# Optimization experiments

Hardware: AMD Instinct MI355X
Metric: run time of the kernel (lower is better)

## Reference

```python
import jax, jax.numpy as jnp
import numpy as np

K_SEL = 8        # selection budget K
R_ITER = 1       # fixed-point refinement steps r
LAM = 0.5        # lam
MAX_PROXY = 16   # max_proxy_points
KNN_K = 1        # knn_k = max(1, r)


def knn_stats(x, k):
    # x: [B,N,D] -> [B,N,4] stats of k nearest-neighbor distances (self excluded)
    sq = jnp.sum(x * x, axis=-1)
    d2 = sq[:, :, None] + sq[:, None, :] - 2.0 * jnp.einsum('bnd,bmd->bnm', x, x)
    n = x.shape[1]
    d2 = d2 + jnp.eye(n, dtype=x.dtype) * 1e9  # mask self-distance
    neg_vals, _ = jax.lax.top_k(-d2, k)        # k smallest distances
    d = jnp.sqrt(jnp.maximum(-neg_vals, 0.0))  # [B,N,k]
    return jnp.stack([d.mean(-1), d.min(-1), d.max(-1), d.std(-1)], axis=-1)


def build_structural(x, selection_weights=None, knn_k=KNN_K):
    feats = jnp.concatenate([x, knn_stats(x, knn_k)], axis=-1)
    if selection_weights is not None:
        feats = jnp.concatenate([feats, selection_weights[..., None]], axis=-1)
    return feats


def feature_similarity(f):
    fn = f / (jnp.linalg.norm(f, axis=-1, keepdims=True) + 1e-8)
    return jnp.einsum('bnd,bmd->bnm', fn, fn)


def soft_selector(saliency, similarity, log_temp):
    # SoftSelectorProxy.forward
    temp = jnp.clip(jnp.exp(log_temp), 0.1, 10.0)
    y = jax.nn.sigmoid((saliency / (2.0 * LAM) - 0.5) / temp)

    def rescale(y):
        budget = jnp.clip(y.sum(axis=1, keepdims=True), 1e-6, None)
        return y * jnp.minimum(K_SEL / budget, 1.0)

    y = rescale(y)
    for _ in range(R_ITER):
        overlap = jnp.einsum('bnm,bm->bn', similarity, y)
        y = rescale(y / (1.0 + overlap))
    return y


def setup_inputs() -> dict:
    key = jax.random.key(0)
    ks = jax.random.split(key, 8)
    B, N, D, H = 8, 2048, 32, 64
    K_LIFT, D_MODEL = 16, 256
    ANCHOR = D + 4  # structural_feature_dim(input_dim, include_selection=False)
    s = 0.02
    return {
        'x': jax.random.normal(ks[0], (B, N, D), dtype=jnp.float32),
        'log_temp': jnp.zeros((), dtype=jnp.float32),  # init_temperature=1.0
        'W1': jax.random.normal(ks[1], (D, H), dtype=jnp.float32) * s,
        'b1': jnp.zeros((H,), dtype=jnp.float32),
        'W2': jax.random.normal(ks[2], (H, 1), dtype=jnp.float32) * s,
        'b2': jnp.zeros((1,), dtype=jnp.float32),
        'mu': jnp.zeros((ANCHOR,), dtype=jnp.float32),
        'sigma': jnp.ones((ANCHOR,), dtype=jnp.float32),
        'Wl': jax.random.normal(ks[3], (ANCHOR, K_LIFT), dtype=jnp.float32) * s,
        'bl': jnp.zeros((K_LIFT,), dtype=jnp.float32),
        'Wp': jax.random.normal(ks[4], (K_LIFT, D_MODEL), dtype=jnp.float32) * s,
        'bp': jnp.zeros((D_MODEL,), dtype=jnp.float32),
    }


def reference(x, log_temp, W1, b1, W2, b2, mu, sigma, Wl, bl, Wp, bp):
    # CausalEventModel: per-point MLP saliency head
    h = jax.nn.relu(jnp.einsum('bnd,dh->bnh', x, W1) + b1)
    saliency = (jnp.einsum('bnh,ho->bno', h, W2) + b2)[..., 0]  # [B,N]

    structural = build_structural(x, selection_weights=saliency)
    similarity = feature_similarity(structural)                  # [B,N,N]
    y_star = soft_selector(saliency, similarity, log_temp)       # [B,N]

    dense = build_structural(x, selection_weights=None)          # [B,N,anchor]
    lifted = jnp.tanh(jnp.einsum('bna,ak->bnk', (dense - mu) / sigma, Wl) + bl)

    N = lifted.shape[1]
    K_eff = min(N, MAX_PROXY)
    _, top_idx = jax.lax.top_k(y_star, K_eff)                    # [B,K_eff]
    cloud = jnp.take_along_axis(lifted, top_idx[..., None], axis=1)  # [B,K_eff,k]
    tokens = jnp.einsum('bkc,cd->bkd', cloud, Wp) + bp           # [B,K_eff,d_model]
    return tokens, y_star
```

## Files before the change

### kernel.cpp

```cpp
#include <hip/hip_runtime.h>
#include <math.h>

#define B 8
#define N 2048
#define DIM 32
#define HID 64
#define KLIFT 16
#define DMODEL 256
#define KPROXY 16
#define KSEL 8.0f

typedef float f32x4 __attribute__((ext_vector_type(4)));
typedef short bf16x8 __attribute__((ext_vector_type(8)));

__device__ inline unsigned short f2bf(float f) {
  unsigned u = __float_as_uint(f);
  unsigned r = (u + 0x7FFFu + ((u >> 16) & 1u)) >> 16;
  return (unsigned short)r;
}
__device__ inline float bf2f(unsigned short s) {
  return __uint_as_float(((unsigned)s) << 16);
}
__device__ inline float clip_temp(float lt) {
  return fminf(fmaxf(expf(lt), 0.1f), 10.f);
}

__global__ __launch_bounds__(256) void k_prep(
    const float* __restrict__ x, const float* __restrict__ W1,
    const float* __restrict__ b1, const float* __restrict__ W2,
    const float* __restrict__ b2, const float* __restrict__ logt,
    float* __restrict__ sal, float* __restrict__ sq,
    unsigned short* __restrict__ Xhi, unsigned short* __restrict__ Xlo,
    float* __restrict__ partials1, unsigned* __restrict__ nnd2) {
  __shared__ float sW1[DIM * HID];
  __shared__ float sW2[HID], sb1[HID];
  __shared__ float red[4];
  int t = threadIdx.x;
  int lane = t & 63, wid = t >> 6;
  {
    const float4* s4 = (const float4*)W1;
    float4* d4 = (float4*)sW1;
    for (int i = t; i < DIM * HID / 4; i += 256) d4[i] = s4[i];
    if (t < HID) { sW2[t] = W2[t]; sb1[t] = b1[t]; }
  }
  __syncthreads();
  int p = blockIdx.x * 256 + t;
  nnd2[p] = 0x7F7F7F7Fu;
  float xr[DIM];
  const float4* xp = (const float4*)(x + (size_t)p * DIM);
#pragma unroll
  for (int i = 0; i < DIM / 4; i++) {
    float4 v = xp[i];
    xr[4 * i + 0] = v.x; xr[4 * i + 1] = v.y; xr[4 * i + 2] = v.z; xr[4 * i + 3] = v.w;
  }
  float s = 0.f;
#pragma unroll
  for (int d = 0; d < DIM; d++) s = fmaf(xr[d], xr[d], s);
  sq[p] = s;
  float h[HID];
#pragma unroll
  for (int j = 0; j < HID; j++) h[j] = sb1[j];
  for (int d = 0; d < DIM; d++) {
    float xv = xr[d];
    const float4* wrow = (const float4*)(&sW1[d * HID]);
#pragma unroll
    for (int j4 = 0; j4 < HID / 4; j4++) {
      float4 w = wrow[j4];
      h[4 * j4 + 0] = fmaf(xv, w.x, h[4 * j4 + 0]);
      h[4 * j4 + 1] = fmaf(xv, w.y, h[4 * j4 + 1]);
      h[4 * j4 + 2] = fmaf(xv, w.z, h[4 * j4 + 2]);
      h[4 * j4 + 3] = fmaf(xv, w.w, h[4 * j4 + 3]);
    }
  }
  float acc = b2[0];
#pragma unroll
  for (int j = 0; j < HID; j++) acc = fmaf(fmaxf(h[j], 0.f), sW2[j], acc);
  sal[p] = acc;
  float temp = clip_temp(logt[0]);
  float y0 = 1.f / (1.f + expf(-((acc - 0.5f) / temp)));
  float part = y0;
#pragma unroll
  for (int off = 32; off >= 1; off >>= 1) part += __shfl_xor(part, off);
  if (lane == 0) red[wid] = part;
  __syncthreads();
  if (t == 0) partials1[blockIdx.x] = red[0] + red[1] + red[2] + red[3];
  int bb = p >> 11, n = p & (N - 1);
  int tile = n >> 4, c = n & 15;
  size_t tb = ((size_t)(bb * 128 + tile)) * 64;
#pragma unroll
  for (int g = 0; g < 4; g++) {
    bf16x8 hv, lv;
#pragma unroll
    for (int j = 0; j < 8; j++) {
      float v = xr[g * 8 + j];
      unsigned short hb = f2bf(v);
      hv[j] = (short)hb;
      lv[j] = (short)f2bf(v - bf2f(hb));
    }
    size_t off = (tb + (size_t)g * 16 + c) * 8;
    *(bf16x8*)(Xhi + off) = hv;
    *(bf16x8*)(Xlo + off) = lv;
  }
}

__global__ __launch_bounds__(256) void k_nnd(
    const unsigned short* __restrict__ Xhi, const unsigned short* __restrict__ Xlo,
    const float* __restrict__ sq, unsigned* __restrict__ nnd2) {
  int bid = blockIdx.x;
  int bb = bid >> 7;
  int nch = (bid >> 3) & 15;
  int mo = bid & 7;
  int t = threadIdx.x;
  int w = t >> 6, lane = t & 63;
  int c = lane & 15, g = lane >> 4;
  __shared__ unsigned short ldsH[16 * 512];
  __shared__ unsigned short ldsL[16 * 512];
  __shared__ float ssq[256];
  {
    size_t base = ((size_t)(bb * 128 + mo * 16)) * 512;
    const float4* srcH = (const float4*)(Xhi + base);
    const float4* srcL = (const float4*)(Xlo + base);
    float4* dH = (float4*)ldsH;
    float4* dL = (float4*)ldsL;
    for (int i = t; i < 1024; i += 256) { dH[i] = srcH[i]; dL[i] = srcL[i]; }
    ssq[t] = sq[bb * N + mo * 256 + t];
  }
  int nt0 = nch * 8 + w * 2, nt1 = nt0 + 1;
  bf16x8 ah0 = *(const bf16x8*)(Xhi + (((size_t)(bb * 128 + nt0)) * 64 + lane) * 8);
  bf16x8 al0 = *(const bf16x8*)(Xlo + (((size_t)(bb * 128 + nt0)) * 64 + lane) * 8);
  bf16x8 ah1 = *(const bf16x8*)(Xhi + (((size_t)(bb * 128 + nt1)) * 64 + lane) * 8);
  bf16x8 al1 = *(const bf16x8*)(Xlo + (((size_t)(bb * 128 + nt1)) * 64 + lane) * 8);
  __syncthreads();
  float mn0[4] = {1e30f, 1e30f, 1e30f, 1e30f};
  float mn1[4] = {1e30f, 1e30f, 1e30f, 1e30f};
  for (int tt = 0; tt < 16; tt++) {
    bf16x8 bh = ((const bf16x8*)(ldsH + tt * 512))[lane];
    bf16x8 bl2 = ((const bf16x8*)(ldsL + tt * 512))[lane];
    f32x4 a0 = {0.f, 0.f, 0.f, 0.f};
    f32x4 a1 = {0.f, 0.f, 0.f, 0.f};
    a0 = __builtin_amdgcn_mfma_f32_16x16x32_bf16(ah0, bh, a0, 0, 0, 0);
    a1 = __builtin_amdgcn_mfma_f32_16x16x32_bf16(ah1, bh, a1, 0, 0, 0);
    a0 = __builtin_amdgcn_mfma_f32_16x16x32_bf16(ah0, bl2, a0, 0, 0, 0);
    a1 = __builtin_amdgcn_mfma_f32_16x16x32_bf16(ah1, bl2, a1, 0, 0, 0);
    a0 = __builtin_amdgcn_mfma_f32_16x16x32_bf16(al0, bh, a0, 0, 0, 0);
    a1 = __builtin_amdgcn_mfma_f32_16x16x32_bf16(al1, bh, a1, 0, 0, 0);
    float sm = ssq[tt * 16 + c];
    int mtg = mo * 16 + tt;
    bool d0 = (mtg == nt0), d1 = (mtg == nt1);
#pragma unroll
    for (int r = 0; r < 4; r++) {
      float v0 = fmaf(-2.f, a0[r], sm);
      float v1 = fmaf(-2.f, a1[r], sm);
      if (d0 && c == 4 * g + r) v0 = 1e30f;
      if (d1 && c == 4 * g + r) v1 = 1e30f;
      mn0[r] = fminf(mn0[r], v0);
      mn1[r] = fminf(mn1[r], v1);
    }
  }
#pragma unroll
  for (int off = 1; off <= 8; off <<= 1) {
#pragma unroll
    for (int r = 0; r < 4; r++) {
      mn0[r] = fminf(mn0[r], __shfl_xor(mn0[r], off));
      mn1[r] = fminf(mn1[r], __shfl_xor(mn1[r], off));
    }
  }
  if (c == 0) {
#pragma unroll
    for (int r = 0; r < 4; r++) {
      int n0 = nt0 * 16 + 4 * g + r;
      float v = fmaxf(sq[bb * N + n0] + mn0[r], 0.f);
      atomicMin(&nnd2[bb * N + n0], __float_as_uint(v));
      int n1 = nt1 * 16 + 4 * g + r;
      v = fmaxf(sq[bb * N + n1] + mn1[r], 0.f);
      atomicMin(&nnd2[bb * N + n1], __float_as_uint(v));
    }
  }
}

__global__ __launch_bounds__(256) void k_c1(
    const float* __restrict__ x, const float* __restrict__ sal,
    const float* __restrict__ sq, const unsigned* __restrict__ nnd2,
    const float* __restrict__ logt, const float* __restrict__ partials1,
    float* __restrict__ gpart) {
  int bid = blockIdx.x;
  int bb = bid >> 3, ch = bid & 7;
  int t = threadIdx.x, lane = t & 63, wid = t >> 6;
  __shared__ float xs[256][33];
  __shared__ float cs[256];
  __shared__ float gsh[8][32];
  __shared__ float red32[4], red33[4];
  int n = ch * 256 + t;
  size_t base = (size_t)bb * N + n;
  float temp = clip_temp(logt[0]);
  float b1v = 0.f;
  for (int j = 0; j < 8; j++) b1v += partials1[bb * 8 + j];
  float scale1 = fminf(KSEL / fmaxf(b1v, 1e-6f), 1.f);
  float sv = sal[base];
  float y0 = 1.f / (1.f + expf(-((sv - 0.5f) / temp)));
  float y1 = y0 * scale1;
  float dv = sqrtf(__uint_as_float(nnd2[base]));
  float nrm = sqrtf(sq[base] + 3.f * dv * dv + sv * sv) + 1e-8f;
  float cn = y1 / nrm;
  cs[t] = cn;
  {
    const float4* xsrc = (const float4*)(x + ((size_t)bb * N + ch * 256) * DIM);
    for (int j = t; j < 2048; j += 256) {
      float4 v = xsrc[j];
      int pt = j >> 3, c4 = (j & 7) * 4;
      xs[pt][c4 + 0] = v.x; xs[pt][c4 + 1] = v.y;
      xs[pt][c4 + 2] = v.z; xs[pt][c4 + 3] = v.w;
    }
  }
  float v32 = cn * dv, v33 = cn * sv;
#pragma unroll
  for (int off = 32; off >= 1; off >>= 1) {
    v32 += __shfl_xor(v32, off);
    v33 += __shfl_xor(v33, off);
  }
  if (lane == 0) { red32[wid] = v32; red33[wid] = v33; }
  __syncthreads();
  if (t == 0) {
    gpart[(size_t)(bb * 8 + ch) * 36 + 32] = red32[0] + red32[1] + red32[2] + red32[3];
    gpart[(size_t)(bb * 8 + ch) * 36 + 33] = red33[0] + red33[1] + red33[2] + red33[3];
  }
  int d = t & 31, pg = t >> 5;
  float acc = 0.f;
#pragma unroll
  for (int i = 0; i < 32; i++) acc = fmaf(cs[pg * 32 + i], xs[pg * 32 + i][d], acc);
  gsh[pg][d] = acc;
  __syncthreads();
  if (t < 32) {
    float s = 0.f;
#pragma unroll
    for (int pgi = 0; pgi < 8; pgi++) s += gsh[pgi][t];
    gpart[(size_t)(bb * 8 + ch) * 36 + t] = s;
  }
}

__global__ __launch_bounds__(256) void k_c(
    const float* __restrict__ x, const float* __restrict__ sal,
    const float* __restrict__ sq, const unsigned* __restrict__ nnd2,
    const float* __restrict__ logt, const float* __restrict__ partials1,
    const float* __restrict__ gpart, float* __restrict__ partials2,
    float* __restrict__ y2buf) {
  int bid = blockIdx.x;
  int bb = bid >> 3, ch = bid & 7;
  int t = threadIdx.x, lane = t & 63, wid = t >> 6;
  __shared__ float gfin[34];
  __shared__ float s1sh;
  __shared__ float red[4];
  if (t < 34) {
    float s = 0.f;
    for (int j = 0; j < 8; j++) s += gpart[(size_t)(bb * 8 + j) * 36 + t];
    gfin[t] = s;
  }
  if (t == 40) {
    float s = 0.f;
    for (int j = 0; j < 8; j++) s += partials1[bb * 8 + j];
    s1sh = fminf(KSEL / fmaxf(s, 1e-6f), 1.f);
  }
  __syncthreads();
  float scale1 = s1sh;
  int n = ch * 256 + t;
  size_t base = (size_t)bb * N + n;
  float temp = clip_temp(logt[0]);
  float sv = sal[base];
  float y0 = 1.f / (1.f + expf(-((sv - 0.5f) / temp)));
  float y1 = y0 * scale1;
  float dv = sqrtf(__uint_as_float(nnd2[base]));
  float nrm = sqrtf(sq[base] + 3.f * dv * dv + sv * sv) + 1e-8f;
  const float4* p4 = (const float4*)(x + base * DIM);
  float ov = 0.f;
#pragma unroll
  for (int cc = 0; cc < 8; cc++) {
    float4 v = p4[cc];
    ov = fmaf(v.x, gfin[4 * cc + 0], ov);
    ov = fmaf(v.y, gfin[4 * cc + 1], ov);
    ov = fmaf(v.z, gfin[4 * cc + 2], ov);
    ov = fmaf(v.w, gfin[4 * cc + 3], ov);
  }
  ov += 3.f * dv * gfin[32] + sv * gfin[33];
  ov /= nrm;
  float y2 = y1 / (1.f + ov);
  y2buf[base] = y2;
  float part = y2;
#pragma unroll
  for (int off = 32; off >= 1; off >>= 1) part += __shfl_xor(part, off);
  if (lane == 0) red[wid] = part;
  __syncthreads();
  if (t == 0) partials2[bb * 8 + ch] = red[0] + red[1] + red[2] + red[3];
}

__global__ __launch_bounds__(256) void k_rank(
    const float* __restrict__ y2buf, const float* __restrict__ partials2,
    float* __restrict__ ystar, int* __restrict__ topidx) {
  int bid = blockIdx.x;
  int bb = bid >> 4, seg = bid & 15;
  int t = threadIdx.x;
  __shared__ float yv[N];
  __shared__ float s2sh;
  if (t == 0) {
    float s = 0.f;
    for (int j = 0; j < 8; j++) s += partials2[bb * 8 + j];
    s2sh = fminf(KSEL / fmaxf(s, 1e-6f), 1.f);
  }
  __syncthreads();
  float scale2 = s2sh;
  size_t base = (size_t)bb * N;
  {
    const float4* src = (const float4*)(y2buf + base);
    float4* dst = (float4*)yv;
#pragma unroll
    for (int i = 0; i < 2; i++) {
      float4 v = src[t + 256 * i];
      v.x *= scale2; v.y *= scale2; v.z *= scale2; v.w *= scale2;
      dst[t + 256 * i] = v;
    }
  }
  __syncthreads();
  int pt = seg * 128 + (t >> 1);
  int h = t & 1;
  float vi = yv[pt];
  if (h == 0) ystar[base + pt] = vi;
  int cnt = 0;
  const float4* yv4 = (const float4*)yv;
  int j0 = h * 256;
#define RCMP(a, q4) { int jb = (q4) * 4; \
    cnt += (a.x > vi || (a.x == vi && jb + 0 < pt)); \
    cnt += (a.y > vi || (a.y == vi && jb + 1 < pt)); \
    cnt += (a.z > vi || (a.z == vi && jb + 2 < pt)); \
    cnt += (a.w > vi || (a.w == vi && jb + 3 < pt)); }
  for (int it = 0; it < 32; it++) {
    int jj = j0 + it * 8;
    float4 a0 = yv4[jj + 0]; float4 a1 = yv4[jj + 1];
    float4 a2 = yv4[jj + 2]; float4 a3 = yv4[jj + 3];
    float4 a4 = yv4[jj + 4]; float4 a5 = yv4[jj + 5];
    float4 a6 = yv4[jj + 6]; float4 a7 = yv4[jj + 7];
    RCMP(a0, jj + 0); RCMP(a1, jj + 1); RCMP(a2, jj + 2); RCMP(a3, jj + 3);
    RCMP(a4, jj + 4); RCMP(a5, jj + 5); RCMP(a6, jj + 6); RCMP(a7, jj + 7);
  }
#undef RCMP
  int oc = __shfl_xor(cnt, 1);
  int tot = cnt + oc;
  if (h == 0 && tot < KPROXY) topidx[bb * KPROXY + tot] = pt;
}

__global__ __launch_bounds__(256) void k_tok(
    const float* __restrict__ x, const unsigned* __restrict__ nnd2,
    const int* __restrict__ topidx, const float* __restrict__ mu,
    const float* __restrict__ sigma, const float* __restrict__ Wl,
    const float* __restrict__ bl, const float* __restrict__ Wp,
    const float* __restrict__ bp, float* __restrict__ tok) {
  int bk = blockIdx.x;
  int b = bk >> 4, k = bk & 15;
  int t = threadIdx.x;
  __shared__ float z[36]; __shared__ float lift[KLIFT]; __shared__ int srow;
  if (t == 0) srow = topidx[b * KPROXY + k];
  __syncthreads();
  int n = srow;
  if (t < 36) {
    float dvv;
    if (t < DIM) dvv = x[((size_t)(b * N + n)) * DIM + t];
    else if (t < 35) dvv = sqrtf(__uint_as_float(nnd2[b * N + n]));
    else dvv = 0.f;
    z[t] = (dvv - mu[t]) / sigma[t];
  }
  __syncthreads();
  if (t < KLIFT) {
    float a = bl[t];
#pragma unroll
    for (int d = 0; d < 36; d++) a = fmaf(z[d], Wl[d * KLIFT + t], a);
    lift[t] = tanhf(a);
  }
  __syncthreads();
  float a = bp[t];
#pragma unroll
  for (int j = 0; j < KLIFT; j++) a = fmaf(lift[j], Wp[j * DMODEL + t], a);
  tok[(size_t)(b * KPROXY + k) * DMODEL + t] = a;
}

extern "C" void kernel_launch(void* const* d_in, const int* in_sizes, int n_in,
                              void* d_out, int out_size, void* d_ws, size_t ws_size,
                              hipStream_t stream) {
  const float* x  = (const float*)d_in[0];
  const float* lt = (const float*)d_in[1];
  const float* W1 = (const float*)d_in[2];
  const float* b1 = (const float*)d_in[3];
  const float* W2 = (const float*)d_in[4];
  const float* b2 = (const float*)d_in[5];
  const float* mu = (const float*)d_in[6];
  const float* sg = (const float*)d_in[7];
  const float* Wl = (const float*)d_in[8];
  const float* bl = (const float*)d_in[9];
  const float* Wp = (const float*)d_in[10];
  const float* bp = (const float*)d_in[11];

  float* tok = (float*)d_out;
  float* ystar = tok + B * KPROXY * DMODEL;

  char* ws = (char*)d_ws;
  float* sal          = (float*)(ws);
  float* sq           = (float*)(ws + 65536);
  unsigned* nnd2      = (unsigned*)(ws + 131072);
  float* y2buf        = (float*)(ws + 196608);
  float* partials1    = (float*)(ws + 262144);
  float* gpart        = (float*)(ws + 262656);
  float* partials2    = (float*)(ws + 272384);
  int* topidx         = (int*)(ws + 272896);
  unsigned short* Xhi = (unsigned short*)(ws + 327680);
  unsigned short* Xlo = (unsigned short*)(ws + 327680 + 1048576);

  k_prep<<<B * N / 256, 256, 0, stream>>>(x, W1, b1, W2, b2, lt, sal, sq, Xhi, Xlo, partials1, nnd2);
  k_nnd<<<B * 16 * 8, 256, 0, stream>>>(Xhi, Xlo, sq, nnd2);
  k_c1<<<B * 8, 256, 0, stream>>>(x, sal, sq, nnd2, lt, partials1, gpart);
  k_c<<<B * 8, 256, 0, stream>>>(x, sal, sq, nnd2, lt, partials1, gpart, partials2, y2buf);
  k_rank<<<B * 16, 256, 0, stream>>>(y2buf, partials2, ystar, topidx);
  k_tok<<<B * KPROXY, 256, 0, stream>>>(x, nnd2, topidx, mu, sg, Wl, bl, Wp, bp, tok);
}
```

Baseline: 63.43 us.

## Fuse four tail kernels into one persistent kernel with grid barriers

New measurement: 109.4 us. +72.4%, slower.

```diff
diff --git a/kernel.cpp b/kernel.cpp
--- a/kernel.cpp
+++ b/kernel.cpp
@@ -9,6 +9,7 @@
 #define DMODEL 256
 #define KPROXY 16
 #define KSEL 8.0f
+#define NBLK 64
 
 typedef float f32x4 __attribute__((ext_vector_type(4)));
 typedef short bf16x8 __attribute__((ext_vector_type(8)));
@@ -23,6 +24,17 @@
 }
 __device__ inline float clip_temp(float lt) {
   return fminf(fmaxf(expf(lt), 0.1f), 10.f);
+}
+
+__device__ inline void grid_barrier(unsigned* ctr, int t) {
+  __syncthreads();
+  if (t == 0) {
+    __threadfence();
+    atomicAdd(ctr, 1u);
+    while (atomicAdd(ctr, 0u) < (unsigned)NBLK) __builtin_amdgcn_s_sleep(4);
+    __threadfence();
+  }
+  __syncthreads();
 }
 
 __global__ __launch_bounds__(256) void k_prep(
@@ -31,12 +43,14 @@
     const float* __restrict__ b2, const float* __restrict__ logt,
     float* __restrict__ sal, float* __restrict__ sq,
     unsigned short* __restrict__ Xhi, unsigned short* __restrict__ Xlo,
-    float* __restrict__ partials1, unsigned* __restrict__ nnd2) {
+    float* __restrict__ partials1, unsigned* __restrict__ nnd2,
+    unsigned* __restrict__ barctr) {
   __shared__ float sW1[DIM * HID];
   __shared__ float sW2[HID], sb1[HID];
   __shared__ float red[4];
   int t = threadIdx.x;
   int lane = t & 63, wid = t >> 6;
+  if (blockIdx.x == 0 && t < 4) barctr[t] = 0u;
   {
     const float4* s4 = (const float4*)W1;
     float4* d4 = (float4*)sW1;
@@ -178,206 +192,206 @@
   }
 }
 
-__global__ __launch_bounds__(256) void k_c1(
+__global__ __launch_bounds__(256) void k_tail(
     const float* __restrict__ x, const float* __restrict__ sal,
     const float* __restrict__ sq, const unsigned* __restrict__ nnd2,
     const float* __restrict__ logt, const float* __restrict__ partials1,
-    float* __restrict__ gpart) {
+    float* __restrict__ gpart, float* __restrict__ partials2,
+    float* __restrict__ y2buf, int* __restrict__ topidx,
+    const float* __restrict__ mu, const float* __restrict__ sigma,
+    const float* __restrict__ Wl, const float* __restrict__ bl,
+    const float* __restrict__ Wp, const float* __restrict__ bp,
+    float* __restrict__ ystar, float* __restrict__ tok,
+    unsigned* __restrict__ barctr) {
   int bid = blockIdx.x;
-  int bb = bid >> 3, ch = bid & 7;
   int t = threadIdx.x, lane = t & 63, wid = t >> 6;
   __shared__ float xs[256][33];
   __shared__ float cs[256];
   __shared__ float gsh[8][32];
   __shared__ float red32[4], red33[4];
-  int n = ch * 256 + t;
-  size_t base = (size_t)bb * N + n;
-  float temp = clip_temp(logt[0]);
-  float b1v = 0.f;
-  for (int j = 0; j < 8; j++) b1v += partials1[bb * 8 + j];
-  float scale1 = fminf(KSEL / fmaxf(b1v, 1e-6f), 1.f);
-  float sv = sal[base];
-  float y0 = 1.f / (1.f + expf(-((sv - 0.5f) / temp)));
-  float y1 = y0 * scale1;
-  float dv = sqrtf(__uint_as_float(nnd2[base]));
-  float nrm = sqrtf(sq[base] + 3.f * dv * dv + sv * sv) + 1e-8f;
-  float cn = y1 / nrm;
-  cs[t] = cn;
-  {
-    const float4* xsrc = (const float4*)(x + ((size_t)bb * N + ch * 256) * DIM);
-    for (int j = t; j < 2048; j += 256) {
-      float4 v = xsrc[j];
-      int pt = j >> 3, c4 = (j & 7) * 4;
-      xs[pt][c4 + 0] = v.x; xs[pt][c4 + 1] = v.y;
-      xs[pt][c4 + 2] = v.z; xs[pt][c4 + 3] = v.w;
-    }
-  }
-  float v32 = cn * dv, v33 = cn * sv;
-#pragma unroll
-  for (int off = 32; off >= 1; off >>= 1) {
-    v32 += __shfl_xor(v32, off);
-    v33 += __shfl_xor(v33, off);
-  }
-  if (lane == 0) { red32[wid] = v32; red33[wid] = v33; }
-  __syncthreads();
-  if (t == 0) {
-    gpart[(size_t)(bb * 8 + ch) * 36 + 32] = red32[0] + red32[1] + red32[2] + red32[3];
-    gpart[(size_t)(bb * 8 + ch) * 36 + 33] = red33[0] + red33[1] + red33[2] + red33[3];
-  }
-  int d = t & 31, pg = t >> 5;
-  float acc = 0.f;
-#pragma unroll
-  for (int i = 0; i < 32; i++) acc = fmaf(cs[pg * 32 + i], xs[pg * 32 + i][d], acc);
-  gsh[pg][d] = acc;
-  __syncthreads();
-  if (t < 32) {
-    float s = 0.f;
-#pragma unroll
-    for (int pgi = 0; pgi < 8; pgi++) s += gsh[pgi][t];
-    gpart[(size_t)(bb * 8 + ch) * 36 + t] = s;
-  }
-}
-
-__global__ __launch_bounds__(256) void k_c(
-    const float* __restrict__ x, const float* __restrict__ sal,
-    const float* __restrict__ sq, const unsigned* __restrict__ nnd2,
-    const float* __restrict__ logt, const float* __restrict__ partials1,
-    const float* __restrict__ gpart, float* __restrict__ partials2,
-    float* __restrict__ y2buf) {
-  int bid = blockIdx.x;
-  int bb = bid >> 3, ch = bid & 7;
-  int t = threadIdx.x, lane = t & 63, wid = t >> 6;
   __shared__ float gfin[34];
   __shared__ float s1sh;
   __shared__ float red[4];
-  if (t < 34) {
-    float s = 0.f;
-    for (int j = 0; j < 8; j++) s += gpart[(size_t)(bb * 8 + j) * 36 + t];
-    gfin[t] = s;
-  }
-  if (t == 40) {
-    float s = 0.f;
-    for (int j = 0; j < 8; j++) s += partials1[bb * 8 + j];
-    s1sh = fminf(KSEL / fmaxf(s, 1e-6f), 1.f);
-  }
-  __syncthreads();
-  float scale1 = s1sh;
-  int n = ch * 256 + t;
-  size_t base = (size_t)bb * N + n;
-  float temp = clip_temp(logt[0]);
-  float sv = sal[base];
-  float y0 = 1.f / (1.f + expf(-((sv - 0.5f) / temp)));
-  float y1 = y0 * scale1;
-  float dv = sqrtf(__uint_as_float(nnd2[base]));
-  float nrm = sqrtf(sq[base] + 3.f * dv * dv + sv * sv) + 1e-8f;
-  const float4* p4 = (const float4*)(x + base * DIM);
-  float ov = 0.f;
-#pragma unroll
-  for (int cc = 0; cc < 8; cc++) {
-    float4 v = p4[cc];
-    ov = fmaf(v.x, gfin[4 * cc + 0], ov);
-    ov = fmaf(v.y, gfin[4 * cc + 1], ov);
-    ov = fmaf(v.z, gfin[4 * cc + 2], ov);
-    ov = fmaf(v.w, gfin[4 * cc + 3], ov);
-  }
-  ov += 3.f * dv * gfin[32] + sv * gfin[33];
-  ov /= nrm;
-  float y2 = y1 / (1.f + ov);
-  y2buf[base] = y2;
-  float part = y2;
-#pragma unroll
-  for (int off = 32; off >= 1; off >>= 1) part += __shfl_xor(part, off);
-  if (lane == 0) red[wid] = part;
-  __syncthreads();
-  if (t == 0) partials2[bb * 8 + ch] = red[0] + red[1] + red[2] + red[3];
-}
-
-__global__ __launch_bounds__(256) void k_rank(
-    const float* __restrict__ y2buf, const float* __restrict__ partials2,
-    float* __restrict__ ystar, int* __restrict__ topidx) {
-  int bid = blockIdx.x;
-  int bb = bid >> 4, seg = bid & 15;
-  int t = threadIdx.x;
   __shared__ float yv[N];
   __shared__ float s2sh;
-  if (t == 0) {
-    float s = 0.f;
-    for (int j = 0; j < 8; j++) s += partials2[bb * 8 + j];
-    s2sh = fminf(KSEL / fmaxf(s, 1e-6f), 1.f);
-  }
-  __syncthreads();
-  float scale2 = s2sh;
-  size_t base = (size_t)bb * N;
+  __shared__ float z[36];
+  __shared__ float lift[KLIFT];
+  __shared__ int srow;
+
+  float temp = clip_temp(logt[0]);
+  int bb = bid >> 3, ch = bid & 7;
+
   {
-    const float4* src = (const float4*)(y2buf + base);
-    float4* dst = (float4*)yv;
-#pragma unroll
-    for (int i = 0; i < 2; i++) {
-      float4 v = src[t + 256 * i];
-      v.x *= scale2; v.y *= scale2; v.z *= scale2; v.w *= scale2;
-      dst[t + 256 * i] = v;
-    }
-  }
-  __syncthreads();
-  int pt = seg * 128 + (t >> 1);
-  int h = t & 1;
-  float vi = yv[pt];
-  if (h == 0) ystar[base + pt] = vi;
-  int cnt = 0;
-  const float4* yv4 = (const float4*)yv;
-  int j0 = h * 256;
+    int n = ch * 256 + t;
+    size_t base = (size_t)bb * N + n;
+    float b1v = 0.f;
+    for (int j = 0; j < 8; j++) b1v += partials1[bb * 8 + j];
+    float scale1 = fminf(KSEL / fmaxf(b1v, 1e-6f), 1.f);
+    float sv = sal[base];
+    float y0 = 1.f / (1.f + expf(-((sv - 0.5f) / temp)));
+    float y1 = y0 * scale1;
+    float dv = sqrtf(__uint_as_float(nnd2[base]));
+    float nrm = sqrtf(sq[base] + 3.f * dv * dv + sv * sv) + 1e-8f;
+    float cn = y1 / nrm;
+    cs[t] = cn;
+    {
+      const float4* xsrc = (const float4*)(x + ((size_t)bb * N + ch * 256) * DIM);
+      for (int j = t; j < 2048; j += 256) {
+        float4 v = xsrc[j];
+        int pt = j >> 3, c4 = (j & 7) * 4;
+        xs[pt][c4 + 0] = v.x; xs[pt][c4 + 1] = v.y;
+        xs[pt][c4 + 2] = v.z; xs[pt][c4 + 3] = v.w;
+      }
+    }
+    float v32 = cn * dv, v33 = cn * sv;
+#pragma unroll
+    for (int off = 32; off >= 1; off >>= 1) {
+      v32 += __shfl_xor(v32, off);
+      v33 += __shfl_xor(v33, off);
+    }
+    if (lane == 0) { red32[wid] = v32; red33[wid] = v33; }
+    __syncthreads();
+    if (t == 0) {
+      gpart[(size_t)(bb * 8 + ch) * 36 + 32] = red32[0] + red32[1] + red32[2] + red32[3];
+      gpart[(size_t)(bb * 8 + ch) * 36 + 33] = red33[0] + red33[1] + red33[2] + red33[3];
+    }
+    int d = t & 31, pg = t >> 5;
+    float acc = 0.f;
+#pragma unroll
+    for (int i = 0; i < 32; i++) acc = fmaf(cs[pg * 32 + i], xs[pg * 32 + i][d], acc);
+    gsh[pg][d] = acc;
+    __syncthreads();
+    if (t < 32) {
+      float s = 0.f;
+#pragma unroll
+      for (int pgi = 0; pgi < 8; pgi++) s += gsh[pgi][t];
+      gpart[(size_t)(bb * 8 + ch) * 36 + t] = s;
+    }
+  }
+  grid_barrier(&barctr[0], t);
+
+  {
+    if (t < 34) {
+      float s = 0.f;
+      for (int j = 0; j < 8; j++) s += gpart[(size_t)(bb * 8 + j) * 36 + t];
+      gfin[t] = s;
+    }
+    if (t == 40) {
+      float s = 0.f;
+      for (int j = 0; j < 8; j++) s += partials1[bb * 8 + j];
+      s1sh = fminf(KSEL / fmaxf(s, 1e-6f), 1.f);
+    }
+    __syncthreads();
+    float scale1 = s1sh;
+    int n = ch * 256 + t;
+    size_t base = (size_t)bb * N + n;
+    float sv = sal[base];
+    float y0 = 1.f / (1.f + expf(-((sv - 0.5f) / temp)));
+    float y1 = y0 * scale1;
+    float dv = sqrtf(__uint_as_float(nnd2[base]));
+    float nrm = sqrtf(sq[base] + 3.f * dv * dv + sv * sv) + 1e-8f;
+    const float4* p4 = (const float4*)(x + base * DIM);
+    float ov = 0.f;
+#pragma unroll
+    for (int cc = 0; cc < 8; cc++) {
+      float4 v = p4[cc];
+      ov = fmaf(v.x, gfin[4 * cc + 0], ov);
+      ov = fmaf(v.y, gfin[4 * cc + 1], ov);
+      ov = fmaf(v.z, gfin[4 * cc + 2], ov);
+      ov = fmaf(v.w, gfin[4 * cc + 3], ov);
+    }
+    ov += 3.f * dv * gfin[32] + sv * gfin[33];
+    ov /= nrm;
+    float y2 = y1 / (1.f + ov);
+    y2buf[base] = y2;
+    float part = y2;
+#pragma unroll
+    for (int off = 32; off >= 1; off >>= 1) part += __shfl_xor(part, off);
+    if (lane == 0) red[wid] = part;
+    __syncthreads();
+    if (t == 0) partials2[bb * 8 + ch] = red[0] + red[1] + red[2] + red[3];
+  }
+  grid_barrier(&barctr[1], t);
+
+  {
+    if (t == 0) {
+      float s = 0.f;
+      for (int j = 0; j < 8; j++) s += partials2[bb * 8 + j];
+      s2sh = fminf(KSEL / fmaxf(s, 1e-6f), 1.f);
+    }
+    __syncthreads();
+    float scale2 = s2sh;
+    size_t base = (size_t)bb * N;
+    {
+      const float4* src = (const float4*)(y2buf + base);
+      float4* dst = (float4*)yv;
+#pragma unroll
+      for (int i = 0; i < 2; i++) {
+        float4 v = src[t + 256 * i];
+        v.x *= scale2; v.y *= scale2; v.z *= scale2; v.w *= scale2;
+        dst[t + 256 * i] = v;
+      }
+    }
+    __syncthreads();
+    const float4* yv4 = (const float4*)yv;
+#pragma unroll
+    for (int sgi = 0; sgi < 2; sgi++) {
+      int seg = ch * 2 + sgi;
+      int pt = seg * 128 + (t >> 1);
+      int h = t & 1;
+      float vi = yv[pt];
+      if (h == 0) ystar[base + pt] = vi;
+      int cnt = 0;
+      int j0 = h * 256;
 #define RCMP(a, q4) { int jb = (q4) * 4; \
-    cnt += (a.x > vi || (a.x == vi && jb + 0 < pt)); \
-    cnt += (a.y > vi || (a.y == vi && jb + 1 < pt)); \
-    cnt += (a.z > vi || (a.z == vi && jb + 2 < pt)); \
-    cnt += (a.w > vi || (a.w == vi && jb + 3 < pt)); }
-  for (int it = 0; it < 32; it++) {
-    int jj = j0 + it * 8;
-    float4 a0 = yv4[jj + 0]; float4 a1 = yv4[jj + 1];
-    float4 a2 = yv4[jj + 2]; float4 a3 = yv4[jj + 3];
-    float4 a4 = yv4[jj + 4]; float4 a5 = yv4[jj + 5];
-    float4 a6 = yv4[jj + 6]; float4 a7 = yv4[jj + 7];
-    RCMP(a0, jj + 0); RCMP(a1, jj + 1); RCMP(a2, jj + 2); RCMP(a3, jj + 3);
-    RCMP(a4, jj + 4); RCMP(a5, jj + 5); RCMP(a6, jj + 6); RCMP(a7, jj + 7);
-  }
+      cnt += (a.x > vi || (a.x == vi && jb + 0 < pt)); \
+      cnt += (a.y > vi || (a.y == vi && jb + 1 < pt)); \
+      cnt += (a.z > vi || (a.z == vi && jb + 2 < pt)); \
+      cnt += (a.w > vi || (a.w == vi && jb + 3 < pt)); }
+      for (int it = 0; it < 32; it++) {
+        int jj = j0 + it * 8;
+        float4 a0 = yv4[jj + 0]; float4 a1 = yv4[jj + 1];
+        float4 a2 = yv4[jj + 2]; float4 a3 = yv4[jj + 3];
+        float4 a4 = yv4[jj + 4]; float4 a5 = yv4[jj + 5];
+        float4 a6 = yv4[jj + 6]; float4 a7 = yv4[jj + 7];
+        RCMP(a0, jj + 0); RCMP(a1, jj + 1); RCMP(a2, jj + 2); RCMP(a3, jj + 3);
+        RCMP(a4, jj + 4); RCMP(a5, jj + 5); RCMP(a6, jj + 6); RCMP(a7, jj + 7);
+      }
 #undef RCMP
-  int oc = __shfl_xor(cnt, 1);
-  int tot = cnt + oc;
-  if (h == 0 && tot < KPROXY) topidx[bb * KPROXY + tot] = pt;
-}
-
-__global__ __launch_bounds__(256) void k_tok(
-    const float* __restrict__ x, const unsigned* __restrict__ nnd2,
-    const int* __restrict__ topidx, const float* __restrict__ mu,
-    const float* __restrict__ sigma, const float* __restrict__ Wl,
-    const float* __restrict__ bl, const float* __restrict__ Wp,
-    const float* __restrict__ bp, float* __restrict__ tok) {
-  int bk = blockIdx.x;
-  int b = bk >> 4, k = bk & 15;
-  int t = threadIdx.x;
-  __shared__ float z[36]; __shared__ float lift[KLIFT]; __shared__ int srow;
-  if (t == 0) srow = topidx[b * KPROXY + k];
-  __syncthreads();
-  int n = srow;
-  if (t < 36) {
-    float dvv;
-    if (t < DIM) dvv = x[((size_t)(b * N + n)) * DIM + t];
-    else if (t < 35) dvv = sqrtf(__uint_as_float(nnd2[b * N + n]));
-    else dvv = 0.f;
-    z[t] = (dvv - mu[t]) / sigma[t];
-  }
-  __syncthreads();
-  if (t < KLIFT) {
-    float a = bl[t];
-#pragma unroll
-    for (int d = 0; d < 36; d++) a = fmaf(z[d], Wl[d * KLIFT + t], a);
-    lift[t] = tanhf(a);
-  }
-  __syncthreads();
-  float a = bp[t];
-#pragma unroll
-  for (int j = 0; j < KLIFT; j++) a = fmaf(lift[j], Wp[j * DMODEL + t], a);
-  tok[(size_t)(b * KPROXY + k) * DMODEL + t] = a;
+      int oc = __shfl_xor(cnt, 1);
+      int tot = cnt + oc;
+      if (h == 0 && tot < KPROXY) topidx[bb * KPROXY + tot] = pt;
+    }
+  }
+  grid_barrier(&barctr[2], t);
+
+  for (int it = 0; it < 2; it++) {
+    int bk = bid * 2 + it;
+    int b = bk >> 4, k = bk & 15;
+    if (t == 0) srow = topidx[b * KPROXY + k];
+    __syncthreads();
+    int n = srow;
+    if (t < 36) {
+      float dvv;
+      if (t < DIM) dvv = x[((size_t)(b * N + n)) * DIM + t];
+      else if (t < 35) dvv = sqrtf(__uint_as_float(nnd2[b * N + n]));
+      else dvv = 0.f;
+      z[t] = (dvv - mu[t]) / sigma[t];
+    }
+    __syncthreads();
+    if (t < KLIFT) {
+      float a = bl[t];
+#pragma unroll
+      for (int d = 0; d < 36; d++) a = fmaf(z[d], Wl[d * KLIFT + t], a);
+      lift[t] = tanhf(a);
+    }
+    __syncthreads();
+    float a = bp[t];
+#pragma unroll
+    for (int j = 0; j < KLIFT; j++) a = fmaf(lift[j], Wp[j * DMODEL + t], a);
+    tok[(size_t)(b * KPROXY + k) * DMODEL + t] = a;
+    __syncthreads();
+  }
 }
 
 extern "C" void kernel_launch(void* const* d_in, const int* in_sizes, int n_in,
@@ -408,13 +422,12 @@
   float* gpart        = (float*)(ws + 262656);
   float* partials2    = (float*)(ws + 272384);
   int* topidx         = (int*)(ws + 272896);
+  unsigned* barctr    = (unsigned*)(ws + 274432);
   unsigned short* Xhi = (unsigned short*)(ws + 327680);
   unsigned short* Xlo = (unsigned short*)(ws + 327680 + 1048576);
 
-  k_prep<<<B * N / 256, 256, 0, stream>>>(x, W1, b1, W2, b2, lt, sal, sq, Xhi, Xlo, partials1, nnd2);
+  k_prep<<<B * N / 256, 256, 0, stream>>>(x, W1, b1, W2, b2, lt, sal, sq, Xhi, Xlo, partials1, nnd2, barctr);
   k_nnd<<<B * 16 * 8, 256, 0, stream>>>(Xhi, Xlo, sq, nnd2);
-  k_c1<<<B * 8, 256, 0, stream>>>(x, sal, sq, nnd2, lt, partials1, gpart);
-  k_c<<<B * 8, 256, 0, stream>>>(x, sal, sq, nnd2, lt, partials1, gpart, partials2, y2buf);
-  k_rank<<<B * 16, 256, 0, stream>>>(y2buf, partials2, ystar, topidx);
-  k_tok<<<B * KPROXY, 256, 0, stream>>>(x, nnd2, topidx, mu, sg, Wl, bl, Wp, bp, tok);
-}
+  k_tail<<<NBLK, 256, 0, stream>>>(x, sal, sq, nnd2, lt, partials1, gpart, partials2,
+                                   y2buf, topidx, mu, sg, Wl, bl, Wp, bp, ystar, tok, barctr);
+}
```
